# Kernel optimization log

Measured on AMD Instinct MI355X. Metric: run time of the kernel, lower is better.

Reference implementation:

```python
import jax, jax.numpy as jnp
import numpy as np

N_NODES = 10000  # static number of graph nodes (segment count)


def setup_inputs() -> dict:
    key = jax.random.key(0)
    ks = jax.random.split(key, 7)
    B, N, DIN, DOUT, E = 2, N_NODES, 256, 256, 320000
    x = jax.random.normal(ks[0], (B, N, DIN), dtype=jnp.float32)
    W = jax.random.normal(ks[1], (DIN, DOUT), dtype=jnp.float32) * (1.0 / np.sqrt(DIN))
    loop_W = jax.random.normal(ks[2], (DIN, DOUT), dtype=jnp.float32) * (1.0 / np.sqrt(DIN))
    bias = jax.random.normal(ks[3], (DOUT,), dtype=jnp.float32) * 0.01
    edge_vals = jax.random.uniform(ks[4], (E,), dtype=jnp.float32)
    rows = jax.random.randint(ks[5], (E,), 0, N, dtype=jnp.int32)
    cols = jax.random.randint(ks[6], (E,), 0, N, dtype=jnp.int32)
    return {"x": x, "W": W, "loop_W": loop_W, "bias": bias,
            "edge_vals": edge_vals, "rows": rows, "cols": cols}


def reference(x, W, loop_W, bias, edge_vals, rows, cols):
    # Dense feature transforms: [b,n,din] @ [din,dout] -> [b,n,dout]
    support = jnp.einsum('bni,io->bno', x, W)
    support_loop = jnp.einsum('bni,io->bno', x, loop_W)
    # Sparse adjacency matmul (COO SpMM): out[r] += val_e * support[:, c_e, :]
    msgs = support[:, cols, :] * edge_vals[None, :, None]      # [b, E, dout]
    agg = jax.ops.segment_sum(
        jnp.swapaxes(msgs, 0, 1), rows, num_segments=N_NODES)   # [n, b, dout]
    agg = jnp.swapaxes(agg, 0, 1)                                # [b, n, dout]
    out = agg + support_loop + bias
    return jax.nn.relu(out)
```

## Files before the change

### kernel.cpp

```cpp
#include <hip/hip_runtime.h>
#include <hip/hip_bf16.h>


#define NN 10000
#define DK 256
#define DO 256
#define MT 20000
#define SCAN_T 1024
#define SCAN_C 10
#define CVB 2500

typedef short short8 __attribute__((ext_vector_type(8)));
typedef float f32x4 __attribute__((ext_vector_type(4)));

#define GLOAD_LDS(G, L) __builtin_amdgcn_global_load_lds(                 \
    (const __attribute__((address_space(1))) void*)(G),                   \
    (__attribute__((address_space(3))) void*)(L), 16, 0, 0)

__device__ inline unsigned short f2bf(float f) {
    unsigned int u = __float_as_uint(f);
    u = (u + 0x7FFFu + ((u >> 16) & 1u)) >> 16;
    return (unsigned short)u;
}
__device__ inline float bf2f(unsigned short s) {
    return __uint_as_float(((unsigned int)s) << 16);
}

__global__ __launch_bounds__(256) void prep_kernel(
    const float* __restrict__ X, unsigned short* __restrict__ Xb,
    const float* __restrict__ W, const float* __restrict__ LW,
    unsigned short* __restrict__ Wt, unsigned short* __restrict__ LWt,
    const int* __restrict__ rows, int* __restrict__ counts, int E)
{
    __shared__ float tile[64][65];
    const int bid = blockIdx.x;
    if (bid < CVB) {
        const int i = bid * 256 + threadIdx.x;
        const float4 a = ((const float4*)X)[2 * i];
        const float4 b = ((const float4*)X)[2 * i + 1];
        short8 o;
        o[0] = (short)f2bf(a.x); o[1] = (short)f2bf(a.y);
        o[2] = (short)f2bf(a.z); o[3] = (short)f2bf(a.w);
        o[4] = (short)f2bf(b.x); o[5] = (short)f2bf(b.y);
        o[6] = (short)f2bf(b.z); o[7] = (short)f2bf(b.w);
        *(short8*)&Xb[(size_t)i * 8] = o;
    } else if (bid < CVB + 32) {
        const int zb = bid - CVB;
        const int z = zb >> 4, rem = zb & 15;
        const int k0 = (rem >> 2) * 64, c0 = (rem & 3) * 64;
        const float* src = z ? LW : W;
        unsigned short* dst = z ? LWt : Wt;
        #pragma unroll
        for (int it = 0; it < 16; ++it) {
            const int u = it * 256 + threadIdx.x;
            const int i = u >> 6, j = u & 63;
            tile[i][j] = src[(size_t)(k0 + i) * DO + c0 + j];
        }
        __syncthreads();
        #pragma unroll
        for (int it = 0; it < 16; ++it) {
            const int u = it * 256 + threadIdx.x;
            const int j = u >> 6, i = u & 63;
            dst[(size_t)(c0 + j) * DK + k0 + i] = f2bf(tile[i][j]);
        }
    } else {
        const int e = (bid - CVB - 32) * 256 + threadIdx.x;
        if (e < E) atomicAdd(&counts[rows[e]], 1);
    }
}

__global__ __launch_bounds__(SCAN_T) void scan_rows(
    const int* __restrict__ counts, int* __restrict__ offsets,
    int* __restrict__ cursor)
{
    __shared__ int sums[SCAN_T];
    const int t = threadIdx.x;
    int local[SCAN_C];
    int s = 0;
    const int base = t * SCAN_C;
    #pragma unroll
    for (int i = 0; i < SCAN_C; ++i) {
        const int idx = base + i;
        const int c = (idx < NN) ? counts[idx] : 0;
        local[i] = s;
        s += c;
    }
    sums[t] = s;
    __syncthreads();
    for (int off = 1; off < SCAN_T; off <<= 1) {
        int u = (t >= off) ? sums[t - off] : 0;
        __syncthreads();
        sums[t] += u;
        __syncthreads();
    }
    const int excl = (t == 0) ? 0 : sums[t - 1];
    #pragma unroll
    for (int i = 0; i < SCAN_C; ++i) {
        const int idx = base + i;
        if (idx < NN) {
            const int o = excl + local[i];
            offsets[idx] = o;
            cursor[idx]  = o;
        }
    }
}

__global__ __launch_bounds__(256) void main_kernel(
    const unsigned short* __restrict__ Xb, const unsigned short* __restrict__ Wt,
    const unsigned short* __restrict__ LWt, const float* __restrict__ bias,
    unsigned short* __restrict__ sup, float* __restrict__ outv,
    const int* __restrict__ rows, const int* __restrict__ cols,
    const float* __restrict__ vals, int* __restrict__ cursor,
    float2* __restrict__ epack, int E, int gemmBlocks)
{
    __shared__ unsigned short Abuf[8 * 64 * 8];
    __shared__ unsigned short BbufW[8 * 64 * 8];
    __shared__ unsigned short BbufL[8 * 64 * 8];

    if ((int)blockIdx.x >= gemmBlocks) {
        const int e = (blockIdx.x - gemmBlocks) * 256 + threadIdx.x;
        if (e < E) {
            const int p = atomicAdd(&cursor[rows[e]], 1);
            epack[p] = make_float2(__int_as_float(cols[e]), vals[e]);
        }
        return;
    }

    const int t = threadIdx.x;
    const int wid = t >> 6, lane = t & 63;
    const int wm = wid >> 1, wn = wid & 1;
    const int m0 = (blockIdx.x >> 2) * 64;
    const int n0 = (blockIdx.x & 3) * 64;

    f32x4 accW[2][2], accL[2][2];
    #pragma unroll
    for (int i = 0; i < 2; ++i)
        #pragma unroll
        for (int j = 0; j < 2; ++j) {
            accW[i][j] = (f32x4){0.f, 0.f, 0.f, 0.f};
            accL[i][j] = (f32x4){0.f, 0.f, 0.f, 0.f};
        }

    for (int k0 = 0; k0 < DK; k0 += 64) {
        #pragma unroll
        for (int c = 0; c < 2; ++c) {
            const int kg = c * 4 + wid;
            const int src_r = lane ^ kg;
            const size_t aoff = (size_t)(m0 + src_r) * DK + k0 + kg * 8;
            const size_t boff = (size_t)(n0 + src_r) * DK + k0 + kg * 8;
            unsigned short* ldst = &Abuf[(c * 256 + wid * 64) * 8];
            GLOAD_LDS(&Xb[aoff], ldst);
            GLOAD_LDS(&Wt[boff],  &BbufW[(c * 256 + wid * 64) * 8]);
            GLOAD_LDS(&LWt[boff], &BbufL[(c * 256 + wid * 64) * 8]);
        }
        __syncthreads();
        #pragma unroll
        for (int s = 0; s < 2; ++s) {
            const int kg = s * 4 + (lane >> 4);
            short8 af[2], bW[2], bL[2];
            #pragma unroll
            for (int i = 0; i < 2; ++i) {
                const int row = wm * 32 + i * 16 + (lane & 15);
                af[i] = *(const short8*)&Abuf[((size_t)kg * 64 + (row ^ kg)) * 8];
            }
            #pragma unroll
            for (int j = 0; j < 2; ++j) {
                const int col = wn * 32 + j * 16 + (lane & 15);
                bW[j] = *(const short8*)&BbufW[((size_t)kg * 64 + (col ^ kg)) * 8];
                bL[j] = *(const short8*)&BbufL[((size_t)kg * 64 + (col ^ kg)) * 8];
            }
            #pragma unroll
            for (int i = 0; i < 2; ++i)
                #pragma unroll
                for (int j = 0; j < 2; ++j) {
                    accW[i][j] = __builtin_amdgcn_mfma_f32_16x16x32_bf16(
                        af[i], bW[j], accW[i][j], 0, 0, 0);
                    accL[i][j] = __builtin_amdgcn_mfma_f32_16x16x32_bf16(
                        af[i], bL[j], accL[i][j], 0, 0, 0);
                }
        }
        __syncthreads();
    }

    const int rbase = m0 + wm * 32;
    const int cbase = n0 + wn * 32;
    #pragma unroll
    for (int i = 0; i < 2; ++i)
        #pragma unroll
        for (int q = 0; q < 4; ++q) {
            const int row = rbase + i * 16 + (lane >> 4) * 4 + q;
            if (row < MT) {
                #pragma unroll
                for (int j = 0; j < 2; ++j) {
                    const int col = cbase + j * 16 + (lane & 15);
                    sup[(size_t)row * DO + col] = f2bf(accW[i][j][q]);
                    outv[(size_t)row * DO + col] = accL[i][j][q] + bias[col];
                }
            }
        }
}

__global__ __launch_bounds__(256) void agg_relu(
    const unsigned short* __restrict__ sup, const float2* __restrict__ epack,
    const int* __restrict__ offsets, const int* __restrict__ counts,
    float* __restrict__ outv)
{
    const int widx = (blockIdx.x * 256 + threadIdx.x) >> 6;
    if (widx >= 2 * NN) return;
    const int lane = threadIdx.x & 63;
    const int b = widx & 1, r = widx >> 1;
    const int d = lane * 4;
    const size_t supb = (size_t)b * NN * DO + d;
    const int start = offsets[r];
    const int deg   = counts[r];

    float a0 = 0.f, a1 = 0.f, a2 = 0.f, a3 = 0.f;
    #pragma unroll 8
    for (int i = 0; i < deg; ++i) {
        const float2 ep = epack[start + i];
        const int col = __float_as_int(ep.x);
        const float v = ep.y;
        const ushort4 s = *(const ushort4*)&sup[supb + (size_t)col * DO];
        a0 += v * bf2f(s.x); a1 += v * bf2f(s.y);
        a2 += v * bf2f(s.z); a3 += v * bf2f(s.w);
    }

    float* o = &outv[((size_t)b * NN + r) * DO + d];
    float4 t4 = *(const float4*)o;
    t4.x = fmaxf(t4.x + a0, 0.f); t4.y = fmaxf(t4.y + a1, 0.f);
    t4.z = fmaxf(t4.z + a2, 0.f); t4.w = fmaxf(t4.w + a3, 0.f);
    *(float4*)o = t4;
}

extern "C" void kernel_launch(void* const* d_in, const int* in_sizes, int n_in,
                              void* d_out, int out_size, void* d_ws, size_t ws_size,
                              hipStream_t stream)
{
    const float* x    = (const float*)d_in[0];
    const float* W    = (const float*)d_in[1];
    const float* LW   = (const float*)d_in[2];
    const float* bias = (const float*)d_in[3];
    const float* ev   = (const float*)d_in[4];
    const int*   rows = (const int*)d_in[5];
    const int*   cols = (const int*)d_in[6];
    float* out = (float*)d_out;

    const int E = in_sizes[4];
    const int EB = (E + 255) / 256;
    const int gemmBlocks = ((MT + 63) / 64) * 4;

    char* wsb = (char*)d_ws;
    unsigned short* Wt    = (unsigned short*)wsb;
    unsigned short* LWt   = (unsigned short*)(wsb + 131072);
    unsigned short* Xb    = (unsigned short*)(wsb + 262144);
    unsigned short* supb  = (unsigned short*)(wsb + 10518528);
    int* counts  = (int*)(wsb + 20758528);
    int* offsets = (int*)(wsb + 20798528);
    int* cursor  = (int*)(wsb + 20838528);
    float2* epack = (float2*)(wsb + 20878528);

    hipMemsetAsync(counts, 0, NN * sizeof(int), stream);

    prep_kernel<<<CVB + 32 + EB, 256, 0, stream>>>(
        x, Xb, W, LW, Wt, LWt, rows, counts, E);
    scan_rows<<<1, SCAN_T, 0, stream>>>(counts, offsets, cursor);
    main_kernel<<<gemmBlocks + EB, 256, 0, stream>>>(
        Xb, Wt, LWt, bias, supb, out, rows, cols, ev, cursor, epack, E, gemmBlocks);

    const int aggBlocks = (2 * NN * 64 + 255) / 256;
    agg_relu<<<aggBlocks, 256, 0, stream>>>(supb, epack, offsets, counts, out);
}
```

Measured before the change: 123.6 us.

## Partition aggregation by feature quarter mapped to XCDs for L2 locality

Result: no change. 124.7 us (+0.9%).

```diff
diff --git a/kernel.cpp b/kernel.cpp
--- a/kernel.cpp
+++ b/kernel.cpp
@@ -148,8 +148,7 @@
             const int src_r = lane ^ kg;
             const size_t aoff = (size_t)(m0 + src_r) * DK + k0 + kg * 8;
             const size_t boff = (size_t)(n0 + src_r) * DK + k0 + kg * 8;
-            unsigned short* ldst = &Abuf[(c * 256 + wid * 64) * 8];
-            GLOAD_LDS(&Xb[aoff], ldst);
+            GLOAD_LDS(&Xb[aoff],  &Abuf[(c * 256 + wid * 64) * 8]);
             GLOAD_LDS(&Wt[boff],  &BbufW[(c * 256 + wid * 64) * 8]);
             GLOAD_LDS(&LWt[boff], &BbufL[(c * 256 + wid * 64) * 8]);
         }
@@ -205,31 +204,34 @@
     const int* __restrict__ offsets, const int* __restrict__ counts,
     float* __restrict__ outv)
 {
-    const int widx = (blockIdx.x * 256 + threadIdx.x) >> 6;
-    if (widx >= 2 * NN) return;
-    const int lane = threadIdx.x & 63;
-    const int b = widx & 1, r = widx >> 1;
-    const int d = lane * 4;
-    const size_t supb = (size_t)b * NN * DO + d;
+    const int bid = blockIdx.x;
+    const int xcd = bid & 7;
+    const int q = xcd >> 1;
+    const int sub = (bid >> 3) * 2 + (xcd & 1);
+    const int wid = threadIdx.x >> 6, lane = threadIdx.x & 63;
+    const int r = sub * 4 + wid;
+    const int bb = lane >> 5;
+    const int f = q * 64 + (lane & 31) * 2;
     const int start = offsets[r];
     const int deg   = counts[r];
-
-    float a0 = 0.f, a1 = 0.f, a2 = 0.f, a3 = 0.f;
+    const size_t supb = (size_t)bb * NN * DO + f;
+
+    float a0 = 0.f, a1 = 0.f;
     #pragma unroll 8
     for (int i = 0; i < deg; ++i) {
         const float2 ep = epack[start + i];
         const int col = __float_as_int(ep.x);
         const float v = ep.y;
-        const ushort4 s = *(const ushort4*)&sup[supb + (size_t)col * DO];
-        a0 += v * bf2f(s.x); a1 += v * bf2f(s.y);
-        a2 += v * bf2f(s.z); a3 += v * bf2f(s.w);
-    }
-
-    float* o = &outv[((size_t)b * NN + r) * DO + d];
-    float4 t4 = *(const float4*)o;
-    t4.x = fmaxf(t4.x + a0, 0.f); t4.y = fmaxf(t4.y + a1, 0.f);
-    t4.z = fmaxf(t4.z + a2, 0.f); t4.w = fmaxf(t4.w + a3, 0.f);
-    *(float4*)o = t4;
+        const ushort2 s = *(const ushort2*)&sup[supb + (size_t)col * DO];
+        a0 += v * bf2f(s.x);
+        a1 += v * bf2f(s.y);
+    }
+
+    float* o = &outv[((size_t)bb * NN + r) * DO + f];
+    float2 t2 = *(const float2*)o;
+    t2.x = fmaxf(t2.x + a0, 0.f);
+    t2.y = fmaxf(t2.y + a1, 0.f);
+    *(float2*)o = t2;
 }
 
 extern "C" void kernel_launch(void* const* d_in, const int* in_sizes, int n_in,
@@ -267,6 +269,5 @@
     main_kernel<<<gemmBlocks + EB, 256, 0, stream>>>(
         Xb, Wt, LWt, bias, supb, out, rows, cols, ev, cursor, epack, E, gemmBlocks);
 
-    const int aggBlocks = (2 * NN * 64 + 255) / 256;
-    agg_relu<<<aggBlocks, 256, 0, stream>>>(supb, epack, offsets, counts, out);
-}
+    agg_relu<<<NN, 256, 0, stream>>>(supb, epack, offsets, counts, out);
+}
```

## Fuse row counting and scan into prep kernel; stage edge lists in LDS for aggregation

Applied to the files above, without the earlier changes.

Result: slower. 187.9 us (+52.0%).

```diff
diff --git a/kernel.cpp b/kernel.cpp
--- a/kernel.cpp
+++ b/kernel.cpp
@@ -6,9 +6,7 @@
 #define DK 256
 #define DO 256
 #define MT 20000
-#define SCAN_T 1024
-#define SCAN_C 10
-#define CVB 2500
+#define ECAP 128
 
 typedef short short8 __attribute__((ext_vector_type(8)));
 typedef float f32x4 __attribute__((ext_vector_type(4)));
@@ -26,16 +24,74 @@
     return __uint_as_float(((unsigned int)s) << 16);
 }
 
-__global__ __launch_bounds__(256) void prep_kernel(
+__global__ __launch_bounds__(1024) void prep_kernel(
     const float* __restrict__ X, unsigned short* __restrict__ Xb,
     const float* __restrict__ W, const float* __restrict__ LW,
     unsigned short* __restrict__ Wt, unsigned short* __restrict__ LWt,
-    const int* __restrict__ rows, int* __restrict__ counts, int E)
-{
+    const int* __restrict__ rows, int* __restrict__ offsets,
+    int* __restrict__ cursor, int E)
+{
+    __shared__ int lds_cnt[NN];
+    __shared__ int sums[1024];
     __shared__ float tile[64][65];
+    const int tid = threadIdx.x;
     const int bid = blockIdx.x;
-    if (bid < CVB) {
-        const int i = bid * 256 + threadIdx.x;
+
+    if (bid == 0) {
+        for (int i = tid; i < NN; i += 1024) lds_cnt[i] = 0;
+        __syncthreads();
+        for (int i = tid; i < E; i += 1024) atomicAdd(&lds_cnt[rows[i]], 1);
+        __syncthreads();
+        int local[10];
+        int s = 0;
+        const int base = tid * 10;
+        #pragma unroll
+        for (int q = 0; q < 10; ++q) {
+            const int idx = base + q;
+            const int c = (idx < NN) ? lds_cnt[idx] : 0;
+            local[q] = s;
+            s += c;
+        }
+        sums[tid] = s;
+        __syncthreads();
+        for (int off = 1; off < 1024; off <<= 1) {
+            int u = (tid >= off) ? sums[tid - off] : 0;
+            __syncthreads();
+            sums[tid] += u;
+            __syncthreads();
+        }
+        const int excl = (tid == 0) ? 0 : sums[tid - 1];
+        #pragma unroll
+        for (int q = 0; q < 10; ++q) {
+            const int idx = base + q;
+            if (idx < NN) {
+                const int o = excl + local[q];
+                offsets[idx] = o;
+                cursor[idx]  = o;
+            }
+        }
+        if (tid == 1023) offsets[NN] = sums[1023];
+    } else if (bid < 33) {
+        const int zb = bid - 1;
+        const int z = zb >> 4, rem = zb & 15;
+        const int k0 = (rem >> 2) * 64, c0 = (rem & 3) * 64;
+        const float* src = z ? LW : W;
+        unsigned short* dst = z ? LWt : Wt;
+        #pragma unroll
+        for (int p = 0; p < 4; ++p) {
+            const int u = p * 1024 + tid;
+            const int i = u >> 6, j = u & 63;
+            tile[i][j] = src[(size_t)(k0 + i) * DO + c0 + j];
+        }
+        __syncthreads();
+        #pragma unroll
+        for (int p = 0; p < 4; ++p) {
+            const int u = p * 1024 + tid;
+            const int j = u >> 6, i = u & 63;
+            dst[(size_t)(c0 + j) * DK + k0 + i] = f2bf(tile[i][j]);
+        }
+    } else {
+        const int i = (bid - 33) * 1024 + tid;
         const float4 a = ((const float4*)X)[2 * i];
         const float4 b = ((const float4*)X)[2 * i + 1];
         short8 o;
@@ -44,64 +100,6 @@
         o[4] = (short)f2bf(b.x); o[5] = (short)f2bf(b.y);
         o[6] = (short)f2bf(b.z); o[7] = (short)f2bf(b.w);
         *(short8*)&Xb[(size_t)i * 8] = o;
-    } else if (bid < CVB + 32) {
-        const int zb = bid - CVB;
-        const int z = zb >> 4, rem = zb & 15;
-        const int k0 = (rem >> 2) * 64, c0 = (rem & 3) * 64;
-        const float* src = z ? LW : W;
-        unsigned short* dst = z ? LWt : Wt;
-        #pragma unroll
-        for (int it = 0; it < 16; ++it) {
-            const int u = it * 256 + threadIdx.x;
-            const int i = u >> 6, j = u & 63;
-            tile[i][j] = src[(size_t)(k0 + i) * DO + c0 + j];
-        }
-        __syncthreads();
-        #pragma unroll
-        for (int it = 0; it < 16; ++it) {
-            const int u = it * 256 + threadIdx.x;
-            const int j = u >> 6, i = u & 63;
-            dst[(size_t)(c0 + j) * DK + k0 + i] = f2bf(tile[i][j]);
-        }
-    } else {
-        const int e = (bid - CVB - 32) * 256 + threadIdx.x;
-        if (e < E) atomicAdd(&counts[rows[e]], 1);
-    }
-}
-
-__global__ __launch_bounds__(SCAN_T) void scan_rows(
-    const int* __restrict__ counts, int* __restrict__ offsets,
-    int* __restrict__ cursor)
-{
-    __shared__ int sums[SCAN_T];
-    const int t = threadIdx.x;
-    int local[SCAN_C];
-    int s = 0;
-    const int base = t * SCAN_C;
-    #pragma unroll
-    for (int i = 0; i < SCAN_C; ++i) {
-        const int idx = base + i;
-        const int c = (idx < NN) ? counts[idx] : 0;
-        local[i] = s;
-        s += c;
-    }
-    sums[t] = s;
-    __syncthreads();
-    for (int off = 1; off < SCAN_T; off <<= 1) {
-        int u = (t >= off) ? sums[t - off] : 0;
-        __syncthreads();
-        sums[t] += u;
-        __syncthreads();
-    }
-    const int excl = (t == 0) ? 0 : sums[t - 1];
-    #pragma unroll
-    for (int i = 0; i < SCAN_C; ++i) {
-        const int idx = base + i;
-        if (idx < NN) {
-            const int o = excl + local[i];
-            offsets[idx] = o;
-            cursor[idx]  = o;
-        }
     }
 }
 
@@ -148,8 +146,7 @@
             const int src_r = lane ^ kg;
             const size_t aoff = (size_t)(m0 + src_r) * DK + k0 + kg * 8;
             const size_t boff = (size_t)(n0 + src_r) * DK + k0 + kg * 8;
-            unsigned short* ldst = &Abuf[(c * 256 + wid * 64) * 8];
-            GLOAD_LDS(&Xb[aoff], ldst);
+            GLOAD_LDS(&Xb[aoff],  &Abuf[(c * 256 + wid * 64) * 8]);
             GLOAD_LDS(&Wt[boff],  &BbufW[(c * 256 + wid * 64) * 8]);
             GLOAD_LDS(&LWt[boff], &BbufL[(c * 256 + wid * 64) * 8]);
         }
@@ -202,27 +199,46 @@
 
 __global__ __launch_bounds__(256) void agg_relu(
     const unsigned short* __restrict__ sup, const float2* __restrict__ epack,
-    const int* __restrict__ offsets, const int* __restrict__ counts,
-    float* __restrict__ outv)
-{
-    const int widx = (blockIdx.x * 256 + threadIdx.x) >> 6;
-    if (widx >= 2 * NN) return;
-    const int lane = threadIdx.x & 63;
-    const int b = widx & 1, r = widx >> 1;
+    const int* __restrict__ offsets, float* __restrict__ outv)
+{
+    __shared__ float2 eps[2][ECAP];
+    const int bid = blockIdx.x;
+    const int tid = threadIdx.x;
+    const int r0 = bid * 2;
+
+    const int start0 = offsets[r0];
+    const int end0   = offsets[r0 + 1];
+    const int end1   = offsets[r0 + 2];
+    const int deg0 = end0 - start0, deg1 = end1 - end0;
+
+    {
+        const int half = tid >> 7;
+        const int idx  = tid & (ECAP - 1);
+        const int st = half ? end0 : start0;
+        const int dg = half ? deg1 : deg0;
+        if (idx < dg) eps[half][idx] = epack[st + idx];
+    }
+    __syncthreads();
+
+    const int wid = tid >> 6, lane = tid & 63;
+    const int b = wid & 1, rsel = wid >> 1;
+    const int r = r0 + rsel;
+    const int start = rsel ? end0 : start0;
+    const int deg   = rsel ? deg1 : deg0;
     const int d = lane * 4;
     const size_t supb = (size_t)b * NN * DO + d;
-    const int start = offsets[r];
-    const int deg   = counts[r];
 
     float a0 = 0.f, a1 = 0.f, a2 = 0.f, a3 = 0.f;
     #pragma unroll 8
     for (int i = 0; i < deg; ++i) {
-        const float2 ep = epack[start + i];
+        const float2 ep = (i < ECAP) ? eps[rsel][i] : epack[start + i];
         const int col = __float_as_int(ep.x);
         const float v = ep.y;
-        const ushort4 s = *(const ushort4*)&sup[supb + (size_t)col * DO];
-        a0 += v * bf2f(s.x); a1 += v * bf2f(s.y);
-        a2 += v * bf2f(s.z); a3 += v * bf2f(s.w);
+        const uint2 s2 = *(const uint2*)&sup[supb + (size_t)col * DO];
+        a0 += v * __uint_as_float(s2.x << 16);
+        a1 += v * __uint_as_float(s2.x & 0xFFFF0000u);
+        a2 += v * __uint_as_float(s2.y << 16);
+        a3 += v * __uint_as_float(s2.y & 0xFFFF0000u);
     }
 
     float* o = &outv[((size_t)b * NN + r) * DO + d];
@@ -254,19 +270,15 @@
     unsigned short* LWt   = (unsigned short*)(wsb + 131072);
     unsigned short* Xb    = (unsigned short*)(wsb + 262144);
     unsigned short* supb  = (unsigned short*)(wsb + 10518528);
-    int* counts  = (int*)(wsb + 20758528);
-    int* offsets = (int*)(wsb + 20798528);
-    int* cursor  = (int*)(wsb + 20838528);
-    float2* epack = (float2*)(wsb + 20878528);
-
-    hipMemsetAsync(counts, 0, NN * sizeof(int), stream);
-
-    prep_kernel<<<CVB + 32 + EB, 256, 0, stream>>>(
-        x, Xb, W, LW, Wt, LWt, rows, counts, E);
-    scan_rows<<<1, SCAN_T, 0, stream>>>(counts, offsets, cursor);
+    int* offsets = (int*)(wsb + 20758528);
+    int* cursor  = (int*)(wsb + 20798592);
+    float2* epack = (float2*)(wsb + 20838592);
+
+    prep_kernel<<<1 + 32 + 625, 1024, 0, stream>>>(
+        x, Xb, W, LW, Wt, LWt, rows, offsets, cursor, E);
+
     main_kernel<<<gemmBlocks + EB, 256, 0, stream>>>(
         Xb, Wt, LWt, bias, supb, out, rows, cols, ev, cursor, epack, E, gemmBlocks);
 
-    const int aggBlocks = (2 * NN * 64 + 255) / 256;
-    agg_relu<<<aggBlocks, 256, 0, stream>>>(supb, epack, offsets, counts, out);
-}
+    agg_relu<<<NN / 2, 256, 0, stream>>>(supb, epack, offsets, out);
+}
```

## Split edge loop across half-waves with wide bf16 loads and batched edge fetch

Applied to the files above, without the earlier changes.

After: 122.0 us. No clear change (-1.3%).

```diff
diff --git a/kernel.cpp b/kernel.cpp
--- a/kernel.cpp
+++ b/kernel.cpp
@@ -21,9 +21,6 @@
     unsigned int u = __float_as_uint(f);
     u = (u + 0x7FFFu + ((u >> 16) & 1u)) >> 16;
     return (unsigned short)u;
-}
-__device__ inline float bf2f(unsigned short s) {
-    return __uint_as_float(((unsigned int)s) << 16);
 }
 
 __global__ __launch_bounds__(256) void prep_kernel(
@@ -103,6 +100,7 @@
             cursor[idx]  = o;
         }
     }
+    if (t == SCAN_T - 1) offsets[NN] = sums[SCAN_T - 1];
 }
 
 __global__ __launch_bounds__(256) void main_kernel(
@@ -148,8 +146,7 @@
             const int src_r = lane ^ kg;
             const size_t aoff = (size_t)(m0 + src_r) * DK + k0 + kg * 8;
             const size_t boff = (size_t)(n0 + src_r) * DK + k0 + kg * 8;
-            unsigned short* ldst = &Abuf[(c * 256 + wid * 64) * 8];
-            GLOAD_LDS(&Xb[aoff], ldst);
+            GLOAD_LDS(&Xb[aoff],  &Abuf[(c * 256 + wid * 64) * 8]);
             GLOAD_LDS(&Wt[boff],  &BbufW[(c * 256 + wid * 64) * 8]);
             GLOAD_LDS(&LWt[boff], &BbufL[(c * 256 + wid * 64) * 8]);
         }
@@ -202,33 +199,63 @@
 
 __global__ __launch_bounds__(256) void agg_relu(
     const unsigned short* __restrict__ sup, const float2* __restrict__ epack,
-    const int* __restrict__ offsets, const int* __restrict__ counts,
-    float* __restrict__ outv)
+    const int* __restrict__ offsets, float* __restrict__ outv)
 {
     const int widx = (blockIdx.x * 256 + threadIdx.x) >> 6;
     if (widx >= 2 * NN) return;
     const int lane = threadIdx.x & 63;
     const int b = widx & 1, r = widx >> 1;
-    const int d = lane * 4;
-    const size_t supb = (size_t)b * NN * DO + d;
+    const int h = lane >> 5;
+    const int c32 = lane & 31;
     const int start = offsets[r];
-    const int deg   = counts[r];
+    const int deg   = offsets[r + 1] - start;
+    const size_t supb = (size_t)b * NN * DO + c32 * 8;
 
     float a0 = 0.f, a1 = 0.f, a2 = 0.f, a3 = 0.f;
-    #pragma unroll 8
-    for (int i = 0; i < deg; ++i) {
-        const float2 ep = epack[start + i];
-        const int col = __float_as_int(ep.x);
-        const float v = ep.y;
-        const ushort4 s = *(const ushort4*)&sup[supb + (size_t)col * DO];
-        a0 += v * bf2f(s.x); a1 += v * bf2f(s.y);
-        a2 += v * bf2f(s.z); a3 += v * bf2f(s.w);
-    }
-
+    float a4 = 0.f, a5 = 0.f, a6 = 0.f, a7 = 0.f;
+
+    for (int c0 = 0; c0 < deg; c0 += 64) {
+        const int cnt = min(64, deg - c0);
+        int   colv = 0;
+        float valv = 0.f;
+        if (lane < cnt) {
+            const float2 e = epack[start + c0 + lane];
+            colv = __float_as_int(e.x);
+            valv = e.y;
+        }
+        #pragma unroll 4
+        for (int j = 0; j < cnt; j += 2) {
+            const int cA  = __builtin_amdgcn_readlane(colv, j);
+            const int vAi = __builtin_amdgcn_readlane(__float_as_int(valv), j);
+            const bool hasB = (j + 1) < cnt;
+            const int cB  = hasB ? __builtin_amdgcn_readlane(colv, j + 1) : cA;
+            const int vBi = hasB ? __builtin_amdgcn_readlane(__float_as_int(valv), j + 1) : 0;
+            const int   c = h ? cB : cA;
+            const float v = __int_as_float(h ? vBi : vAi);
+            const uint4 s4 = *(const uint4*)&sup[supb + (size_t)c * DO];
+            a0 += v * __uint_as_float(s4.x << 16);
+            a1 += v * __uint_as_float(s4.x & 0xFFFF0000u);
+            a2 += v * __uint_as_float(s4.y << 16);
+            a3 += v * __uint_as_float(s4.y & 0xFFFF0000u);
+            a4 += v * __uint_as_float(s4.z << 16);
+            a5 += v * __uint_as_float(s4.z & 0xFFFF0000u);
+            a6 += v * __uint_as_float(s4.w << 16);
+            a7 += v * __uint_as_float(s4.w & 0xFFFF0000u);
+        }
+    }
+
+    a0 += __shfl_xor(a0, 32); a1 += __shfl_xor(a1, 32);
+    a2 += __shfl_xor(a2, 32); a3 += __shfl_xor(a3, 32);
+    a4 += __shfl_xor(a4, 32); a5 += __shfl_xor(a5, 32);
+    a6 += __shfl_xor(a6, 32); a7 += __shfl_xor(a7, 32);
+
+    const int d = c32 * 8 + h * 4;
+    const float w0 = h ? a4 : a0, w1 = h ? a5 : a1;
+    const float w2 = h ? a6 : a2, w3 = h ? a7 : a3;
     float* o = &outv[((size_t)b * NN + r) * DO + d];
     float4 t4 = *(const float4*)o;
-    t4.x = fmaxf(t4.x + a0, 0.f); t4.y = fmaxf(t4.y + a1, 0.f);
-    t4.z = fmaxf(t4.z + a2, 0.f); t4.w = fmaxf(t4.w + a3, 0.f);
+    t4.x = fmaxf(t4.x + w0, 0.f); t4.y = fmaxf(t4.y + w1, 0.f);
+    t4.z = fmaxf(t4.z + w2, 0.f); t4.w = fmaxf(t4.w + w3, 0.f);
     *(float4*)o = t4;
 }
 
@@ -256,8 +283,8 @@
     unsigned short* supb  = (unsigned short*)(wsb + 10518528);
     int* counts  = (int*)(wsb + 20758528);
     int* offsets = (int*)(wsb + 20798528);
-    int* cursor  = (int*)(wsb + 20838528);
-    float2* epack = (float2*)(wsb + 20878528);
+    int* cursor  = (int*)(wsb + 20838592);
+    float2* epack = (float2*)(wsb + 20878592);
 
     hipMemsetAsync(counts, 0, NN * sizeof(int), stream);
 
@@ -267,6 +294,5 @@
     main_kernel<<<gemmBlocks + EB, 256, 0, stream>>>(
         Xb, Wt, LWt, bias, supb, out, rows, cols, ev, cursor, epack, E, gemmBlocks);
 
-    const int aggBlocks = (2 * NN * 64 + 255) / 256;
-    agg_relu<<<aggBlocks, 256, 0, stream>>>(supb, epack, offsets, counts, out);
-}
+    agg_relu<<<(2 * NN * 64) / 256, 256, 0, stream>>>(supb, epack, offsets, out);
+}
```
